# Kernel optimization log

Measured on AMD Instinct MI355X. Metric: run time of the kernel, lower is better.

Reference implementation:

```python
import jax, jax.numpy as jnp
import numpy as np

WS = (7, 7)          # window size
SS = (3, 3)          # shift size
HP, WP = 112, 112    # patch grid H, W
C = 128              # embedding dim
NH = 8               # heads
HD = C // NH
SCALE = HD ** -0.5
N = WS[0] * WS[1]    # tokens per window = 49
B = 32


def _rel_index():
    ch = np.arange(WS[0]); cw = np.arange(WS[1])
    coords = np.stack(np.meshgrid(ch, cw, indexing='ij')).reshape(2, -1)
    rel = coords[:, :, None] - coords[:, None, :]
    rel = rel.transpose(1, 2, 0).copy()
    rel[..., 0] += WS[0] - 1
    rel[..., 1] += WS[1] - 1
    rel[..., 0] *= 2 * WS[1] - 1
    return rel.sum(-1)  # [N, N] int


def _attn_mask():
    img = np.zeros((HP, WP))
    hs = [slice(0, -WS[0]), slice(-WS[0], -SS[0]), slice(-SS[0], None)]
    ws = [slice(0, -WS[1]), slice(-WS[1], -SS[1]), slice(-SS[1], None)]
    cnt = 0
    for h in hs:
        for w in ws:
            img[h, w] = cnt
            cnt += 1
    mw = img.reshape(HP // WS[0], WS[0], WP // WS[1], WS[1]).transpose(0, 2, 1, 3).reshape(-1, N)
    am = mw[:, None, :] - mw[:, :, None]
    return np.where(am != 0, -100.0, 0.0).astype(np.float32)  # [nW, N, N]


REL_IDX = jnp.asarray(_rel_index())
ATTN_MASK = jnp.asarray(_attn_mask())


def _window_partition(x):
    b, h, w, c = x.shape
    x = x.reshape(b, h // WS[0], WS[0], w // WS[1], WS[1], c)
    return x.transpose(0, 1, 3, 2, 4, 5).reshape(-1, N, c)


def _window_reverse(win, h, w):
    c = win.shape[-1]
    x = win.reshape(-1, h // WS[0], w // WS[1], WS[0], WS[1], c)
    return x.transpose(0, 1, 3, 2, 4, 5).reshape(-1, h, w, c)


def _layernorm(x, w, b):
    mu = x.mean(-1, keepdims=True)
    var = x.var(-1, keepdims=True)
    return (x - mu) / jnp.sqrt(var + 1e-5) * w + b


def setup_inputs() -> dict:
    key = jax.random.key(0)
    ks = jax.random.split(key, 8)
    s = 0.02
    return {
        'x': jax.random.normal(ks[0], (B, HP, WP, C), jnp.float32),
        'qkv_w': jax.random.normal(ks[1], (C, 3 * C), jnp.float32) * s,
        'qkv_b': jnp.zeros((3 * C,), jnp.float32),
        'proj_w': jax.random.normal(ks[2], (C, C), jnp.float32) * s,
        'proj_b': jnp.zeros((C,), jnp.float32),
        'rpb': jax.random.normal(ks[3], ((2 * WS[0] - 1) * (2 * WS[1] - 1), NH), jnp.float32) * s,
        'ln1_w': jnp.ones((C,), jnp.float32),
        'ln1_b': jnp.zeros((C,), jnp.float32),
        'ln2_w': jnp.ones((C,), jnp.float32),
        'ln2_b': jnp.zeros((C,), jnp.float32),
        'w1': jax.random.normal(ks[4], (C, 4 * C), jnp.float32) * s,
        'b1': jnp.zeros((4 * C,), jnp.float32),
        'w2': jax.random.normal(ks[5], (4 * C, C), jnp.float32) * s,
        'b2': jnp.zeros((C,), jnp.float32),
    }


def reference(x, qkv_w, qkv_b, proj_w, proj_b, rpb, ln1_w, ln1_b, ln2_w, ln2_b, w1, b1, w2, b2):
    b, h, w, c = x.shape
    # NOTE: original code overwrites x with norm1(x), so the residual uses the
    # normed tensor -- reproduced faithfully here.
    xn = _layernorm(x, ln1_w, ln1_b)
    shifted = jnp.roll(xn, (-SS[0], -SS[1]), axis=(1, 2))
    xw = _window_partition(shifted)                      # [B*nW, N, C]
    qkv = xw @ qkv_w + qkv_b                             # [B*nW, N, 3C]
    qkv = qkv.reshape(-1, N, 3, NH, HD).transpose(2, 0, 3, 1, 4)
    q, k, v = qkv[0], qkv[1], qkv[2]                     # [B*nW, NH, N, HD]
    attn = jnp.einsum('bhnd,bhmd->bhnm', q * SCALE, k)   # [B*nW, NH, N, N]
    bias = rpb[REL_IDX].transpose(2, 0, 1)               # [NH, N, N]
    attn = attn + bias[None]
    n_w = ATTN_MASK.shape[0]
    attn = attn.reshape(b, n_w, NH, N, N) + ATTN_MASK[None, :, None]
    attn = jax.nn.softmax(attn.reshape(-1, NH, N, N), axis=-1)
    out = jnp.einsum('bhnm,bhmd->bhnd', attn, v)
    out = out.transpose(0, 2, 1, 3).reshape(-1, N, c)
    out = out @ proj_w + proj_b
    shifted = _window_reverse(out, h, w)
    shifted = jnp.roll(shifted, (SS[0], SS[1]), axis=(1, 2))
    y = xn + shifted
    hid = _layernorm(y, ln2_w, ln2_b)
    hid = jax.nn.gelu(hid @ w1 + b1) @ w2 + b2
    return y + hid
```

## Files before the change

### kernel.cpp

```cpp
#include <hip/hip_runtime.h>
#include <hip/hip_bf16.h>

#define DI __device__ __forceinline__

typedef unsigned short u16;
typedef unsigned int   u32;
typedef float  f32x4  __attribute__((ext_vector_type(4)));
typedef __bf16 bf16x8 __attribute__((ext_vector_type(8)));
typedef u16    us8    __attribute__((ext_vector_type(8)));

DI u16 f2bf(float f){
  u32 u = __builtin_bit_cast(u32, f);
  u = (u + 0x7fffu + ((u >> 16) & 1u)) >> 16;
  return (u16)u;
}
DI float bf2f(u16 h){
  u32 u = ((u32)h) << 16;
  return __builtin_bit_cast(float, u);
}

DI f32x4 mfma16(bf16x8 a, bf16x8 b, f32x4 c){
  return __builtin_amdgcn_mfma_f32_16x16x32_bf16(a, b, c, 0, 0, 0);
}
DI bf16x8 bzero(){
  us8 z = {0,0,0,0,0,0,0,0};
  return __builtin_bit_cast(bf16x8, z);
}
DI bf16x8 ld8s(const u16* p){ return *(const bf16x8*)p; }

__global__ void prep_kernel(const float* __restrict__ qkv_w, const float* __restrict__ proj_w,
                            const float* __restrict__ w1,    const float* __restrict__ w2,
                            const float* __restrict__ rpb,
                            u16* __restrict__ qkvwT, u16* __restrict__ projwT,
                            u16* __restrict__ w1T,   u16* __restrict__ w2T,
                            float* __restrict__ biasC)
{
  const int idx = blockIdx.x * blockDim.x + threadIdx.x;
  const int stride = gridDim.x * blockDim.x;
  for (int i = idx; i < 384*128; i += stride){ int o = i >> 7, k = i & 127; qkvwT[i] = f2bf(qkv_w[k*384 + o]); }
  for (int i = idx; i < 128*128; i += stride){ int o = i >> 7, k = i & 127; projwT[i] = f2bf(proj_w[k*128 + o]); }
  for (int i = idx; i < 512*128; i += stride){ int o = i >> 7, k = i & 127; w1T[i] = f2bf(w1[k*512 + o]); }
  for (int i = idx; i < 128*512; i += stride){ int o = i >> 9, k = i & 511; w2T[i] = f2bf(w2[k*128 + o]); }
  for (int i = idx; i < 4*8*64*64; i += stride){
    const int cls = i >> 15;
    const int rem = i & 32767;
    const int h = rem >> 12;
    const int km = rem & 4095;
    const int key = km >> 6, q = km & 63;
    float v;
    if (key >= 49) v = -1e30f;
    else if (q >= 49) v = 0.f;
    else {
      const int rel = (q/7 - key/7 + 6)*13 + (q%7 - key%7 + 6);
      v = rpb[rel*8 + h];
      const int rhF = cls >> 1, rwF = cls & 1;
      const int labq = (rhF ? ((q/7)   < 4 ? 1 : 2) : 0)*3 + (rwF ? ((q%7)   < 4 ? 1 : 2) : 0);
      const int labk = (rhF ? ((key/7) < 4 ? 1 : 2) : 0)*3 + (rwF ? ((key%7) < 4 ? 1 : 2) : 0);
      if (labq != labk) v -= 100.f;
    }
    biasC[i] = v;
  }
}

__global__ __launch_bounds__(256, 3) void attn_kernel(
    const float* __restrict__ x,
    const float* __restrict__ ln1w, const float* __restrict__ ln1b,
    const float* __restrict__ qkv_b, const float* __restrict__ proj_b,
    const u16* __restrict__ qkvwT, const u16* __restrict__ projwT,
    const float* __restrict__ biasC,
    float* __restrict__ y)
{
  __shared__ u16 qkPool[2*64*136];
  __shared__ u16 pool[128*72];

  u16* qB = qkPool;
  u16* kB = qkPool + 64*136;
  u16* xw = pool;
  float* aoS = (float*)qkPool;

  const int tid = threadIdx.x;
  const int lane = tid & 63;
  const int wv = tid >> 6;
  const int l15 = lane & 15;
  const int lq  = lane >> 4;
  const int blk = blockIdx.x;
  const int b  = blk >> 8;
  const int wi = blk & 255;
  const int wh = wi >> 4, ww = wi & 15;
  const int cls = ((wh == 15) ? 2 : 0) + ((ww == 15) ? 1 : 0);
  const int t = tid >> 2, g = tid & 3;

  u32 xnp[16];

  {
    float vals[32];
    float sum = 0.f, sq = 0.f;
    if (t < 49){
      const int r = t / 7, c = t % 7;
      const int hs   = (wh*7 + r + 3) % 112;
      const int wsrc = (ww*7 + c + 3) % 112;
      const float* src = x + ((size_t)((b*112 + hs)*112 + wsrc))*128 + g*32;
      #pragma unroll
      for (int j = 0; j < 8; j++){
        f32x4 v4 = *(const f32x4*)(src + 4*j);
        vals[4*j+0]=v4[0]; vals[4*j+1]=v4[1]; vals[4*j+2]=v4[2]; vals[4*j+3]=v4[3];
        sum += v4[0] + v4[1] + v4[2] + v4[3];
        sq  += v4[0]*v4[0] + v4[1]*v4[1] + v4[2]*v4[2] + v4[3]*v4[3];
      }
    } else {
      #pragma unroll
      for (int j = 0; j < 32; j++) vals[j] = 0.f;
    }
    sum += __shfl_xor(sum, 1); sum += __shfl_xor(sum, 2);
    sq  += __shfl_xor(sq, 1);  sq  += __shfl_xor(sq, 2);
    const float mu = sum * (1.f/128.f);
    const float var = sq * (1.f/128.f) - mu*mu;
    const float rs = rsqrtf(var + 1e-5f);
    #pragma unroll
    for (int j = 0; j < 32; j++){
      const int ch = g*32 + j;
      float xn = 0.f;
      if (t < 49) xn = (vals[j] - mu) * rs * ln1w[ch] + ln1b[ch];
      const u16 h = f2bf(xn);
      xw[(t*128 + ch) ^ ((t & 7) << 3)] = h;
      if (j & 1) xnp[j >> 1] |= ((u32)h << 16);
      else       xnp[j >> 1]  = (u32)h;
    }
  }
  __syncthreads();

  {
    const f32x4 fz = {0.f,0.f,0.f,0.f};
    f32x4 acc[4][6];
    #pragma unroll
    for (int mt = 0; mt < 4; mt++)
      #pragma unroll
      for (int nt = 0; nt < 6; nt++) acc[mt][nt] = fz;

    const int col0 = wv * 96;
    #pragma unroll
    for (int kk = 0; kk < 4; kk++){
      const int k0 = kk*32 + (lq << 3);
      bf16x8 a[4];
      #pragma unroll
      for (int mt = 0; mt < 4; mt++){
        const int row = mt*16 + l15;
        a[mt] = ld8s(&xw[(row*128 + k0) ^ ((row & 7) << 3)]);
      }
      #pragma unroll
      for (int nt = 0; nt < 6; nt++){
        const int o = col0 + nt*16 + l15;
        const bf16x8 bb = *(const bf16x8*)(qkvwT + o*128 + k0);
        #pragma unroll
        for (int mt = 0; mt < 4; mt++)
          acc[mt][nt] = mfma16(a[mt], bb, acc[mt][nt]);
      }
    }
    __syncthreads();
    #pragma unroll
    for (int nt = 0; nt < 6; nt++){
      const int o = col0 + nt*16 + l15;
      const int which = o >> 7;
      const int ch = o & 127;
      const float bias = qkv_b[o];
      #pragma unroll
      for (int mt = 0; mt < 4; mt++){
        #pragma unroll
        for (int r = 0; r < 4; r++){
          const int tok = mt*16 + (lq << 2) + r;
          const float v = acc[mt][nt][r] + bias;
          if (which == 0)      qB[tok*136 + ch] = f2bf(v * 0.25f);
          else if (which == 1) kB[tok*136 + ch] = f2bf(v);
          else                 pool[ch*72 + tok] = f2bf(v);
        }
      }
    }
  }
  __syncthreads();

  {
    const f32x4 fz = {0.f,0.f,0.f,0.f};
    const int iq = wv*16 + l15;
    const float* bC = biasC + cls*32768 + iq;
    #pragma unroll 1
    for (int hb = 0; hb < 2; hb++){
      float p[4][4][4];
      #pragma unroll
      for (int hh = 0; hh < 4; hh++){
        const int h = hb*4 + hh;
        const bf16x8 bq = (lq < 2) ? ld8s(&qB[iq*136 + h*16 + (lq << 3)]) : bzero();
        const float* bh = bC + h*4096;
        #pragma unroll
        for (int nt = 0; nt < 4; nt++){
          const int keyb = nt*16 + (lq << 2);
          f32x4 cf;
          cf[0] = bh[(keyb+0)*64];
          cf[1] = bh[(keyb+1)*64];
          cf[2] = bh[(keyb+2)*64];
          cf[3] = bh[(keyb+3)*64];
          const bf16x8 ak = (lq < 2) ? ld8s(&kB[(nt*16 + l15)*136 + h*16 + (lq << 3)]) : bzero();
          const f32x4 s4 = mfma16(ak, bq, cf);
          #pragma unroll
          for (int r = 0; r < 4; r++) p[hh][nt][r] = s4[r];
        }
      }
      #pragma unroll
      for (int hh = 0; hh < 4; hh++){
        float m = -3e38f;
        #pragma unroll
        for (int nt = 0; nt < 4; nt++)
          #pragma unroll
          for (int r = 0; r < 4; r++) m = fmaxf(m, p[hh][nt][r]);
        m = fmaxf(m, __shfl_xor(m, 16));
        m = fmaxf(m, __shfl_xor(m, 32));
        float sum = 0.f;
        #pragma unroll
        for (int nt = 0; nt < 4; nt++)
          #pragma unroll
          for (int r = 0; r < 4; r++){
            const float e = __expf(p[hh][nt][r] - m);
            p[hh][nt][r] = e;
            sum += e;
          }
        sum += __shfl_xor(sum, 16);
        sum += __shfl_xor(sum, 32);
        const float inv = 1.f / sum;
        #pragma unroll
        for (int nt = 0; nt < 4; nt++)
          #pragma unroll
          for (int r = 0; r < 4; r++) p[hh][nt][r] *= inv;
      }
      f32x4 oaccb[4];
      #pragma unroll
      for (int hh = 0; hh < 4; hh++){
        const int h = hb*4 + hh;
        bf16x8 pa[2];
        #pragma unroll
        for (int kk = 0; kk < 2; kk++){
          us8 tmp;
          #pragma unroll
          for (int j = 0; j < 8; j++){
            const int srcLane = ((((lq << 1) + (j >> 2)) & 3) << 4) + l15;
            const float va = __shfl(p[hh][2*kk    ][j & 3], srcLane);
            const float vb = __shfl(p[hh][2*kk + 1][j & 3], srcLane);
            tmp[j] = f2bf((lq & 2) ? vb : va);
          }
          pa[kk] = __builtin_bit_cast(bf16x8, tmp);
        }
        f32x4 oacc = fz;
        #pragma unroll
        for (int kk = 0; kk < 2; kk++){
          const bf16x8 bv = ld8s(&pool[(h*16 + l15)*72 + kk*32 + (lq << 3)]);
          oacc = mfma16(pa[kk], bv, oacc);
        }
        oaccb[hh] = oacc;
      }
      __syncthreads();
      #pragma unroll
      for (int hh = 0; hh < 4; hh++){
        const int h = hb*4 + hh;
        #pragma unroll
        for (int r = 0; r < 4; r++){
          const int tok = wv*16 + (lq << 2) + r;
          kB[tok*136 + h*16 + l15] = f2bf(oaccb[hh][r]);
        }
      }
    }
  }
  __syncthreads();

  {
    const f32x4 fz = {0.f,0.f,0.f,0.f};
    f32x4 acc[4][2];
    #pragma unroll
    for (int mt = 0; mt < 4; mt++){ acc[mt][0] = fz; acc[mt][1] = fz; }
    #pragma unroll
    for (int kk = 0; kk < 4; kk++){
      const int k0 = kk*32 + (lq << 3);
      bf16x8 a[4];
      #pragma unroll
      for (int mt = 0; mt < 4; mt++){
        const int row = mt*16 + l15;
        a[mt] = ld8s(&kB[row*136 + k0]);
      }
      #pragma unroll
      for (int nt = 0; nt < 2; nt++){
        const int o = wv*32 + nt*16 + l15;
        const bf16x8 bb = *(const bf16x8*)(projwT + o*128 + k0);
        #pragma unroll
        for (int mt = 0; mt < 4; mt++)
          acc[mt][nt] = mfma16(a[mt], bb, acc[mt][nt]);
      }
    }
    __syncthreads();
    #pragma unroll
    for (int nt = 0; nt < 2; nt++){
      const int ch = wv*32 + nt*16 + l15;
      const float pb = proj_b[ch];
      #pragma unroll
      for (int mt = 0; mt < 4; mt++){
        #pragma unroll
        for (int r = 0; r < 4; r++){
          const int tok = mt*16 + (lq << 2) + r;
          aoS[(tok*128 + ch) ^ ((tok & 7) << 2)] = acc[mt][nt][r] + pb;
        }
      }
    }
  }
  __syncthreads();

  if (t < 49){
    const int rr = t / 7, cc = t % 7;
    const int hs   = (wh*7 + rr + 3) % 112;
    const int wsrc = (ww*7 + cc + 3) % 112;
    float* dst = y + ((size_t)((b*112 + hs)*112 + wsrc))*128 + g*32;
    #pragma unroll
    for (int j = 0; j < 8; j++){
      const int idx = (t*128 + g*32 + 4*j) ^ ((t & 7) << 2);
      const f32x4 a4 = *(const f32x4*)(aoS + idx);
      f32x4 o4;
      #pragma unroll
      for (int e = 0; e < 4; e++){
        const int c = 4*j + e;
        const u16 h = (u16)(xnp[c >> 1] >> ((c & 1) * 16));
        o4[e] = bf2f(h) + a4[e];
      }
      *(f32x4*)(dst + 4*j) = o4;
    }
  }
}

__global__ __launch_bounds__(256, 2) void mlp_kernel(
    const float* __restrict__ ln2w, const float* __restrict__ ln2b,
    const float* __restrict__ b1, const float* __restrict__ b2,
    const u16* __restrict__ w1T, const u16* __restrict__ w2T,
    float* __restrict__ y)
{
  __shared__ u16 yn[128*128];
  __shared__ u16 hid[128*128];
  const int tid = threadIdx.x;
  const int lane = tid & 63;
  const int wv = tid >> 6;
  const int l15 = lane & 15;
  const int lq  = lane >> 4;
  const size_t base = (size_t)blockIdx.x * 128;
  const f32x4 fz = {0.f,0.f,0.f,0.f};

  {
    const int t2 = tid >> 1, gh = tid & 1;
    const float* src = y + (base + t2)*128 + gh*64;
    float vals[64];
    float sum = 0.f, sq = 0.f;
    #pragma unroll
    for (int j = 0; j < 16; j++){
      f32x4 v4 = *(const f32x4*)(src + 4*j);
      vals[4*j+0]=v4[0]; vals[4*j+1]=v4[1]; vals[4*j+2]=v4[2]; vals[4*j+3]=v4[3];
      sum += v4[0] + v4[1] + v4[2] + v4[3];
      sq  += v4[0]*v4[0] + v4[1]*v4[1] + v4[2]*v4[2] + v4[3]*v4[3];
    }
    sum += __shfl_xor(sum, 1);
    sq  += __shfl_xor(sq, 1);
    const float mu = sum * (1.f/128.f);
    const float rs = rsqrtf(sq * (1.f/128.f) - mu*mu + 1e-5f);
    #pragma unroll
    for (int j = 0; j < 64; j++){
      const int ch = gh*64 + j;
      yn[(t2*128 + ch) ^ ((t2 & 7) << 3)] = f2bf((vals[j] - mu) * rs * ln2w[ch] + ln2b[ch]);
    }
  }
  __syncthreads();

  f32x4 acc2[8][2];
  #pragma unroll
  for (int mt = 0; mt < 8; mt++){ acc2[mt][0] = fz; acc2[mt][1] = fz; }

  #pragma unroll 1
  for (int pass = 0; pass < 4; pass++){
    bf16x8 bb1[4][2];
    #pragma unroll
    for (int kk = 0; kk < 4; kk++){
      const int k0 = kk*32 + (lq << 3);
      #pragma unroll
      for (int nt = 0; nt < 2; nt++){
        const int o = pass*128 + wv*32 + nt*16 + l15;
        bb1[kk][nt] = *(const bf16x8*)(w1T + o*128 + k0);
      }
    }
    f32x4 acc[8][2];
    #pragma unroll
    for (int mt = 0; mt < 8; mt++){ acc[mt][0] = fz; acc[mt][1] = fz; }
    #pragma unroll
    for (int kk = 0; kk < 4; kk++){
      const int k0 = kk*32 + (lq << 3);
      bf16x8 a[8];
      #pragma unroll
      for (int mt = 0; mt < 8; mt++){
        const int row = mt*16 + l15;
        a[mt] = ld8s(&yn[(row*128 + k0) ^ ((row & 7) << 3)]);
      }
      #pragma unroll
      for (int nt = 0; nt < 2; nt++)
        #pragma unroll
        for (int mt = 0; mt < 8; mt++)
          acc[mt][nt] = mfma16(a[mt], bb1[kk][nt], acc[mt][nt]);
    }
    bf16x8 bb2[4][2];
    #pragma unroll
    for (int kk = 0; kk < 4; kk++){
      const int k0 = kk*32 + (lq << 3);
      #pragma unroll
      for (int nt = 0; nt < 2; nt++){
        const int o = wv*32 + nt*16 + l15;
        bb2[kk][nt] = *(const bf16x8*)(w2T + o*512 + pass*128 + k0);
      }
    }
    if (pass > 0) __syncthreads();
    #pragma unroll
    for (int nt = 0; nt < 2; nt++){
      const int o = pass*128 + wv*32 + nt*16 + l15;
      const int cl = wv*32 + nt*16 + l15;
      const float bb1s = b1[o];
      #pragma unroll
      for (int mt = 0; mt < 8; mt++){
        #pragma unroll
        for (int r = 0; r < 4; r++){
          const int tok = mt*16 + (lq << 2) + r;
          const float v = acc[mt][nt][r] + bb1s;
          const float u = 0.7978845608028654f * (v + 0.044715f * v*v*v);
          const float th = 1.f - 2.f / (__expf(2.f*u) + 1.f);
          const float gel = 0.5f * v * (1.f + th);
          hid[(tok*128 + cl) ^ ((tok & 7) << 3)] = f2bf(gel);
        }
      }
    }
    __syncthreads();

    #pragma unroll
    for (int kk = 0; kk < 4; kk++){
      const int k0 = kk*32 + (lq << 3);
      bf16x8 a[8];
      #pragma unroll
      for (int mt = 0; mt < 8; mt++){
        const int row = mt*16 + l15;
        a[mt] = ld8s(&hid[(row*128 + k0) ^ ((row & 7) << 3)]);
      }
      #pragma unroll
      for (int nt = 0; nt < 2; nt++)
        #pragma unroll
        for (int mt = 0; mt < 8; mt++)
          acc2[mt][nt] = mfma16(a[mt], bb2[kk][nt], acc2[mt][nt]);
    }
  }

  #pragma unroll
  for (int nt = 0; nt < 2; nt++){
    const int ch = wv*32 + nt*16 + l15;
    const float bb2s = b2[ch];
    #pragma unroll
    for (int mt = 0; mt < 8; mt++){
      #pragma unroll
      for (int r = 0; r < 4; r++){
        const int tok = mt*16 + (lq << 2) + r;
        const size_t gi = (base + tok)*128 + ch;
        y[gi] = y[gi] + acc2[mt][nt][r] + bb2s;
      }
    }
  }
}

extern "C" void kernel_launch(void* const* d_in, const int* in_sizes, int n_in,
                              void* d_out, int out_size, void* d_ws, size_t ws_size,
                              hipStream_t stream)
{
  const float* x      = (const float*)d_in[0];
  const float* qkv_w  = (const float*)d_in[1];
  const float* qkv_b  = (const float*)d_in[2];
  const float* proj_w = (const float*)d_in[3];
  const float* proj_b = (const float*)d_in[4];
  const float* rpb    = (const float*)d_in[5];
  const float* ln1w   = (const float*)d_in[6];
  const float* ln1b   = (const float*)d_in[7];
  const float* ln2w   = (const float*)d_in[8];
  const float* ln2b   = (const float*)d_in[9];
  const float* w1     = (const float*)d_in[10];
  const float* b1     = (const float*)d_in[11];
  const float* w2     = (const float*)d_in[12];
  const float* b2     = (const float*)d_in[13];

  char* ws = (char*)d_ws;
  u16*   qkvwT  = (u16*)(ws + 0);
  u16*   projwT = (u16*)(ws + 98304);
  u16*   w1T    = (u16*)(ws + 131072);
  u16*   w2T    = (u16*)(ws + 262144);
  float* biasC  = (float*)(ws + 393216);
  float* y = (float*)d_out;

  prep_kernel<<<512, 256, 0, stream>>>(qkv_w, proj_w, w1, w2, rpb,
                                       qkvwT, projwT, w1T, w2T, biasC);
  attn_kernel<<<8192, 256, 0, stream>>>(x, ln1w, ln1b, qkv_b, proj_b,
                                        qkvwT, projwT, biasC, y);
  mlp_kernel<<<3136, 256, 0, stream>>>(ln2w, ln2b, b1, b2, w1T, w2T, y);
}
```

Measured before the change: 1.126 ms.

## Shrink MLP hidden chunk to raise occupancy, prefetch weights in attention GEMMs

The MLP kernel now processes the 512-wide hidden layer in eight 64-column passes instead of four 128-column passes. This halves the hid shared buffer and the per-pass accumulator registers, so launch bounds can be raised to 3 blocks per CU. In the attention kernel, QKV weight fragments are software-prefetched one k-step ahead, and proj weights are all loaded before the MMA loop to hide global latency. The trade-off is more passes and barriers in the MLP, plus more live registers in the attention kernel.

```diff
diff --git a/kernel.cpp b/kernel.cpp
--- a/kernel.cpp
+++ b/kernel.cpp
@@ -138,6 +138,10 @@
       for (int nt = 0; nt < 6; nt++) acc[mt][nt] = fz;
 
     const int col0 = wv * 96;
+    bf16x8 bbv[6];
+    #pragma unroll
+    for (int nt = 0; nt < 6; nt++)
+      bbv[nt] = *(const bf16x8*)(qkvwT + (col0 + nt*16 + l15)*128 + (lq << 3));
     #pragma unroll
     for (int kk = 0; kk < 4; kk++){
       const int k0 = kk*32 + (lq << 3);
@@ -147,13 +151,21 @@
         const int row = mt*16 + l15;
         a[mt] = ld8s(&xw[(row*128 + k0) ^ ((row & 7) << 3)]);
       }
-      #pragma unroll
-      for (int nt = 0; nt < 6; nt++){
-        const int o = col0 + nt*16 + l15;
-        const bf16x8 bb = *(const bf16x8*)(qkvwT + o*128 + k0);
+      bf16x8 bbn[6];
+      if (kk < 3){
+        const int k1 = (kk+1)*32 + (lq << 3);
+        #pragma unroll
+        for (int nt = 0; nt < 6; nt++)
+          bbn[nt] = *(const bf16x8*)(qkvwT + (col0 + nt*16 + l15)*128 + k1);
+      }
+      #pragma unroll
+      for (int nt = 0; nt < 6; nt++)
         #pragma unroll
         for (int mt = 0; mt < 4; mt++)
-          acc[mt][nt] = mfma16(a[mt], bb, acc[mt][nt]);
+          acc[mt][nt] = mfma16(a[mt], bbv[nt], acc[mt][nt]);
+      if (kk < 3){
+        #pragma unroll
+        for (int nt = 0; nt < 6; nt++) bbv[nt] = bbn[nt];
       }
     }
     __syncthreads();
@@ -271,6 +283,14 @@
 
   {
     const f32x4 fz = {0.f,0.f,0.f,0.f};
+    bf16x8 pw[4][2];
+    #pragma unroll
+    for (int kk = 0; kk < 4; kk++){
+      const int k0 = kk*32 + (lq << 3);
+      #pragma unroll
+      for (int nt = 0; nt < 2; nt++)
+        pw[kk][nt] = *(const bf16x8*)(projwT + (wv*32 + nt*16 + l15)*128 + k0);
+    }
     f32x4 acc[4][2];
     #pragma unroll
     for (int mt = 0; mt < 4; mt++){ acc[mt][0] = fz; acc[mt][1] = fz; }
@@ -284,13 +304,10 @@
         a[mt] = ld8s(&kB[row*136 + k0]);
       }
       #pragma unroll
-      for (int nt = 0; nt < 2; nt++){
-        const int o = wv*32 + nt*16 + l15;
-        const bf16x8 bb = *(const bf16x8*)(projwT + o*128 + k0);
+      for (int nt = 0; nt < 2; nt++)
         #pragma unroll
         for (int mt = 0; mt < 4; mt++)
-          acc[mt][nt] = mfma16(a[mt], bb, acc[mt][nt]);
-      }
+          acc[mt][nt] = mfma16(a[mt], pw[kk][nt], acc[mt][nt]);
     }
     __syncthreads();
     #pragma unroll
@@ -330,14 +347,14 @@
   }
 }
 
-__global__ __launch_bounds__(256, 2) void mlp_kernel(
+__global__ __launch_bounds__(256, 3) void mlp_kernel(
     const float* __restrict__ ln2w, const float* __restrict__ ln2b,
     const float* __restrict__ b1, const float* __restrict__ b2,
     const u16* __restrict__ w1T, const u16* __restrict__ w2T,
     float* __restrict__ y)
 {
   __shared__ u16 yn[128*128];
-  __shared__ u16 hid[128*128];
+  __shared__ u16 hid[128*64];
   const int tid = threadIdx.x;
   const int lane = tid & 63;
   const int wv = tid >> 6;
@@ -375,20 +392,15 @@
   for (int mt = 0; mt < 8; mt++){ acc2[mt][0] = fz; acc2[mt][1] = fz; }
 
   #pragma unroll 1
-  for (int pass = 0; pass < 4; pass++){
-    bf16x8 bb1[4][2];
-    #pragma unroll
-    for (int kk = 0; kk < 4; kk++){
-      const int k0 = kk*32 + (lq << 3);
-      #pragma unroll
-      for (int nt = 0; nt < 2; nt++){
-        const int o = pass*128 + wv*32 + nt*16 + l15;
-        bb1[kk][nt] = *(const bf16x8*)(w1T + o*128 + k0);
-      }
-    }
-    f32x4 acc[8][2];
-    #pragma unroll
-    for (int mt = 0; mt < 8; mt++){ acc[mt][0] = fz; acc[mt][1] = fz; }
+  for (int pass = 0; pass < 8; pass++){
+    bf16x8 bb1[4];
+    const int oc = pass*64 + wv*16 + l15;
+    #pragma unroll
+    for (int kk = 0; kk < 4; kk++)
+      bb1[kk] = *(const bf16x8*)(w1T + oc*128 + kk*32 + (lq << 3));
+    f32x4 acc[8];
+    #pragma unroll
+    for (int mt = 0; mt < 8; mt++) acc[mt] = fz;
     #pragma unroll
     for (int kk = 0; kk < 4; kk++){
       const int k0 = kk*32 + (lq << 3);
@@ -399,56 +411,45 @@
         a[mt] = ld8s(&yn[(row*128 + k0) ^ ((row & 7) << 3)]);
       }
       #pragma unroll
-      for (int nt = 0; nt < 2; nt++)
-        #pragma unroll
-        for (int mt = 0; mt < 8; mt++)
-          acc[mt][nt] = mfma16(a[mt], bb1[kk][nt], acc[mt][nt]);
-    }
-    bf16x8 bb2[4][2];
-    #pragma unroll
-    for (int kk = 0; kk < 4; kk++){
-      const int k0 = kk*32 + (lq << 3);
-      #pragma unroll
-      for (int nt = 0; nt < 2; nt++){
-        const int o = wv*32 + nt*16 + l15;
-        bb2[kk][nt] = *(const bf16x8*)(w2T + o*512 + pass*128 + k0);
-      }
+      for (int mt = 0; mt < 8; mt++)
+        acc[mt] = mfma16(a[mt], bb1[kk], acc[mt]);
     }
     if (pass > 0) __syncthreads();
-    #pragma unroll
-    for (int nt = 0; nt < 2; nt++){
-      const int o = pass*128 + wv*32 + nt*16 + l15;
-      const int cl = wv*32 + nt*16 + l15;
-      const float bb1s = b1[o];
+    {
+      const int cl = wv*16 + l15;
+      const float bb1s = b1[oc];
       #pragma unroll
       for (int mt = 0; mt < 8; mt++){
         #pragma unroll
         for (int r = 0; r < 4; r++){
           const int tok = mt*16 + (lq << 2) + r;
-          const float v = acc[mt][nt][r] + bb1s;
+          const float v = acc[mt][r] + bb1s;
           const float u = 0.7978845608028654f * (v + 0.044715f * v*v*v);
           const float th = 1.f - 2.f / (__expf(2.f*u) + 1.f);
           const float gel = 0.5f * v * (1.f + th);
-          hid[(tok*128 + cl) ^ ((tok & 7) << 3)] = f2bf(gel);
+          hid[(tok*64 + cl) ^ ((tok & 7) << 3)] = f2bf(gel);
         }
       }
     }
     __syncthreads();
 
     #pragma unroll
-    for (int kk = 0; kk < 4; kk++){
+    for (int kk = 0; kk < 2; kk++){
       const int k0 = kk*32 + (lq << 3);
       bf16x8 a[8];
       #pragma unroll
       for (int mt = 0; mt < 8; mt++){
         const int row = mt*16 + l15;
-        a[mt] = ld8s(&hid[(row*128 + k0) ^ ((row & 7) << 3)]);
-      }
-      #pragma unroll
-      for (int nt = 0; nt < 2; nt++)
+        a[mt] = ld8s(&hid[(row*64 + k0) ^ ((row & 7) << 3)]);
+      }
+      #pragma unroll
+      for (int nt = 0; nt < 2; nt++){
+        const int o = wv*32 + nt*16 + l15;
+        const bf16x8 bb = *(const bf16x8*)(w2T + o*512 + pass*64 + k0);
         #pragma unroll
         for (int mt = 0; mt < 8; mt++)
-          acc2[mt][nt] = mfma16(a[mt], bb2[kk][nt], acc2[mt][nt]);
+          acc2[mt][nt] = mfma16(a[mt], bb, acc2[mt][nt]);
+      }
     }
   }
 
```

Measured after the change: 1.168 ms. +3.7%, slower.

## Prefetch weight fragments into registers and stage MLP output through LDS for vector stores

Applied to the files above, without the earlier changes.

The attention kernel now software-prefetches the next k-slice of QKV weights while the current slice's MFMAs run, and loads all proj weight fragments up front. The MLP kernel preloads W1 fragments for the next pass early. Its epilogue keeps the loaded y row in registers and stages the results through shared memory, so each thread writes a contiguous row with float4 stores instead of a strided read-modify-write of global y. The cost is higher register pressure (vals[64] kept live across the loop, extra weight fragments), which could reduce occupancy.

```diff
diff --git a/kernel.cpp b/kernel.cpp
--- a/kernel.cpp
+++ b/kernel.cpp
@@ -138,6 +138,10 @@
       for (int nt = 0; nt < 6; nt++) acc[mt][nt] = fz;
 
     const int col0 = wv * 96;
+    bf16x8 bbv[6];
+    #pragma unroll
+    for (int nt = 0; nt < 6; nt++)
+      bbv[nt] = *(const bf16x8*)(qkvwT + (col0 + nt*16 + l15)*128 + (lq << 3));
     #pragma unroll
     for (int kk = 0; kk < 4; kk++){
       const int k0 = kk*32 + (lq << 3);
@@ -147,13 +151,21 @@
         const int row = mt*16 + l15;
         a[mt] = ld8s(&xw[(row*128 + k0) ^ ((row & 7) << 3)]);
       }
-      #pragma unroll
-      for (int nt = 0; nt < 6; nt++){
-        const int o = col0 + nt*16 + l15;
-        const bf16x8 bb = *(const bf16x8*)(qkvwT + o*128 + k0);
+      bf16x8 bbn[6];
+      if (kk < 3){
+        const int k1 = (kk+1)*32 + (lq << 3);
+        #pragma unroll
+        for (int nt = 0; nt < 6; nt++)
+          bbn[nt] = *(const bf16x8*)(qkvwT + (col0 + nt*16 + l15)*128 + k1);
+      }
+      #pragma unroll
+      for (int nt = 0; nt < 6; nt++)
         #pragma unroll
         for (int mt = 0; mt < 4; mt++)
-          acc[mt][nt] = mfma16(a[mt], bb, acc[mt][nt]);
+          acc[mt][nt] = mfma16(a[mt], bbv[nt], acc[mt][nt]);
+      if (kk < 3){
+        #pragma unroll
+        for (int nt = 0; nt < 6; nt++) bbv[nt] = bbn[nt];
       }
     }
     __syncthreads();
@@ -271,6 +283,14 @@
 
   {
     const f32x4 fz = {0.f,0.f,0.f,0.f};
+    bf16x8 pw[4][2];
+    #pragma unroll
+    for (int kk = 0; kk < 4; kk++){
+      const int k0 = kk*32 + (lq << 3);
+      #pragma unroll
+      for (int nt = 0; nt < 2; nt++)
+        pw[kk][nt] = *(const bf16x8*)(projwT + (wv*32 + nt*16 + l15)*128 + k0);
+    }
     f32x4 acc[4][2];
     #pragma unroll
     for (int mt = 0; mt < 4; mt++){ acc[mt][0] = fz; acc[mt][1] = fz; }
@@ -284,13 +304,10 @@
         a[mt] = ld8s(&kB[row*136 + k0]);
       }
       #pragma unroll
-      for (int nt = 0; nt < 2; nt++){
-        const int o = wv*32 + nt*16 + l15;
-        const bf16x8 bb = *(const bf16x8*)(projwT + o*128 + k0);
+      for (int nt = 0; nt < 2; nt++)
         #pragma unroll
         for (int mt = 0; mt < 4; mt++)
-          acc[mt][nt] = mfma16(a[mt], bb, acc[mt][nt]);
-      }
+          acc[mt][nt] = mfma16(a[mt], pw[kk][nt], acc[mt][nt]);
     }
     __syncthreads();
     #pragma unroll
@@ -345,11 +362,11 @@
   const int lq  = lane >> 4;
   const size_t base = (size_t)blockIdx.x * 128;
   const f32x4 fz = {0.f,0.f,0.f,0.f};
-
+  const int t2 = tid >> 1, gh = tid & 1;
+
+  float vals[64];
   {
-    const int t2 = tid >> 1, gh = tid & 1;
     const float* src = y + (base + t2)*128 + gh*64;
-    float vals[64];
     float sum = 0.f, sq = 0.f;
     #pragma unroll
     for (int j = 0; j < 16; j++){
@@ -374,18 +391,15 @@
   #pragma unroll
   for (int mt = 0; mt < 8; mt++){ acc2[mt][0] = fz; acc2[mt][1] = fz; }
 
+  bf16x8 bb1[4][2];
+  #pragma unroll
+  for (int kk = 0; kk < 4; kk++)
+    #pragma unroll
+    for (int nt = 0; nt < 2; nt++)
+      bb1[kk][nt] = *(const bf16x8*)(w1T + (wv*32 + nt*16 + l15)*128 + kk*32 + (lq << 3));
+
   #pragma unroll 1
   for (int pass = 0; pass < 4; pass++){
-    bf16x8 bb1[4][2];
-    #pragma unroll
-    for (int kk = 0; kk < 4; kk++){
-      const int k0 = kk*32 + (lq << 3);
-      #pragma unroll
-      for (int nt = 0; nt < 2; nt++){
-        const int o = pass*128 + wv*32 + nt*16 + l15;
-        bb1[kk][nt] = *(const bf16x8*)(w1T + o*128 + k0);
-      }
-    }
     f32x4 acc[8][2];
     #pragma unroll
     for (int mt = 0; mt < 8; mt++){ acc[mt][0] = fz; acc[mt][1] = fz; }
@@ -406,13 +420,17 @@
     }
     bf16x8 bb2[4][2];
     #pragma unroll
-    for (int kk = 0; kk < 4; kk++){
-      const int k0 = kk*32 + (lq << 3);
-      #pragma unroll
-      for (int nt = 0; nt < 2; nt++){
-        const int o = wv*32 + nt*16 + l15;
-        bb2[kk][nt] = *(const bf16x8*)(w2T + o*512 + pass*128 + k0);
-      }
+    for (int kk = 0; kk < 4; kk++)
+      #pragma unroll
+      for (int nt = 0; nt < 2; nt++)
+        bb2[kk][nt] = *(const bf16x8*)(w2T + (wv*32 + nt*16 + l15)*512 + pass*128 + kk*32 + (lq << 3));
+    const int bcol = pass*128 + b1[0]*0;
+    if (pass < 3){
+      #pragma unroll
+      for (int kk = 0; kk < 4; kk++)
+        #pragma unroll
+        for (int nt = 0; nt < 2; nt++)
+          bb1[kk][nt] = *(const bf16x8*)(w1T + ((pass+1)*128 + wv*32 + nt*16 + l15)*128 + kk*32 + (lq << 3));
     }
     if (pass > 0) __syncthreads();
     #pragma unroll
@@ -451,18 +469,39 @@
           acc2[mt][nt] = mfma16(a[mt], bb2[kk][nt], acc2[mt][nt]);
     }
   }
-
-  #pragma unroll
-  for (int nt = 0; nt < 2; nt++){
-    const int ch = wv*32 + nt*16 + l15;
-    const float bb2s = b2[ch];
-    #pragma unroll
-    for (int mt = 0; mt < 8; mt++){
-      #pragma unroll
-      for (int r = 0; r < 4; r++){
-        const int tok = mt*16 + (lq << 2) + r;
-        const size_t gi = (base + tok)*128 + ch;
-        y[gi] = y[gi] + acc2[mt][nt][r] + bb2s;
+  __syncthreads();
+
+  float* hidf = (float*)hid;
+  #pragma unroll 1
+  for (int c = 0; c < 2; c++){
+    if (c) __syncthreads();
+    #pragma unroll
+    for (int nt = 0; nt < 2; nt++){
+      const int ch = wv*32 + nt*16 + l15;
+      const float bb2s = b2[ch];
+      #pragma unroll
+      for (int mtl = 0; mtl < 4; mtl++){
+        const int mt = c*4 + mtl;
+        #pragma unroll
+        for (int r = 0; r < 4; r++){
+          const int tokl = mtl*16 + (lq << 2) + r;
+          hidf[(tokl*128 + ch) ^ ((tokl & 7) << 2)] = acc2[mt][nt][r] + bb2s;
+        }
+      }
+    }
+    __syncthreads();
+    if (t2 >= c*64 && t2 < c*64 + 64){
+      const int tl = t2 - c*64;
+      float* dst = y + (base + t2)*128 + gh*64;
+      #pragma unroll
+      for (int j = 0; j < 16; j++){
+        f32x4 o4;
+        #pragma unroll
+        for (int e = 0; e < 4; e++){
+          const int cc = gh*64 + 4*j + e;
+          o4[e] = vals[4*j + e] + hidf[(tl*128 + cc) ^ ((tl & 7) << 2)];
+        }
+        *(f32x4*)(dst + 4*j) = o4;
       }
     }
   }
```

Measured after the change: 1.592 ms. 41.4% more time.
